# Performance work log

Hardware: AMD Instinct MI355X
Metric: run time of the kernel (lower is better)

Reference implementation:

```python
import jax, jax.numpy as jnp
import numpy as np


def setup_inputs() -> dict:
    key = jax.random.key(0)
    k1, k2 = jax.random.split(key)
    B, C, H, W = 8, 64, 64, 64
    x = jax.random.normal(k1, (B, C, H, W), dtype=jnp.float32)
    stdv = 1.0 / np.sqrt(C)
    weight = jax.random.uniform(k2, (C, C), dtype=jnp.float32, minval=-stdv, maxval=stdv)
    return {"x": x, "weight": weight}


def reference(x, weight):
    B, C, H, W = x.shape
    N = H * W
    xf = x.reshape(B, C, N)            # [B, C, N]
    g_x = jnp.transpose(xf, (0, 2, 1))  # [B, N, C] (also theta_x)
    # f[b, i, j] = sum_c x[b, c, i] * x[b, c, j]
    f = jnp.einsum('bic,bcj->bij', g_x, xf)  # [B, N, N]
    adj = jax.nn.softmax(f, axis=-1)
    support = jnp.einsum('bnc,cd->bnd', g_x, weight)  # [B, N, C]
    y = jnp.einsum('bij,bjc->bic', adj, support)      # [B, N, C]
    y = jnp.transpose(y, (0, 2, 1)).reshape(B, C, H, W)
    return y + x
```

## Files before the change

### kernel.cpp

```cpp
#include <hip/hip_runtime.h>
#include <stdint.h>


#define NTOK 4096
#define CCH  64

typedef float v4f __attribute__((ext_vector_type(4)));
typedef __bf16 v8bf __attribute__((ext_vector_type(8)));
typedef unsigned short v8us __attribute__((ext_vector_type(8)));

__device__ __forceinline__ unsigned short f2bf(float f) {
    union { float f; unsigned int u; } c; c.f = f;
    unsigned int r = c.u + 0x7fffu + ((c.u >> 16) & 1u);
    return (unsigned short)(r >> 16);
}

__device__ __forceinline__ v8bf ld8(const unsigned short* p) {
    union { v8us s; v8bf b; } u;
    u.s = *(const v8us*)p;
    return u.b;
}

__device__ __forceinline__ unsigned int pkbf(float a, float b) {
    union { float f; unsigned int u; } ua, ub; ua.f = a; ub.f = b;
    return __builtin_amdgcn_perm(ub.u, ua.u, 0x07060302u);
}

__device__ __forceinline__ void gload_lds16(const void* g, void* l) {
    __builtin_amdgcn_global_load_lds(
        (const __attribute__((address_space(1))) unsigned int*)g,
        (__attribute__((address_space(3))) unsigned int*)l,
        16, 0, 0);
}

__global__ __launch_bounds__(256) void prep_kernel(
    const float* __restrict__ x,
    const float* __restrict__ w,
    unsigned short* __restrict__ xT,
    unsigned short* __restrict__ sT)
{
    __shared__ float Xf[64 * 65];

    const int tid  = threadIdx.x;
    const int lane = tid & 63;
    const int wv   = __builtin_amdgcn_readfirstlane(tid >> 6);
    const int b    = blockIdx.y;
    const int n0   = blockIdx.x * 64;

    const float* xb = x + (size_t)b * CCH * NTOK + n0 + lane;
    #pragma unroll
    for (int k = 0; k < 16; ++k) {
        const int c = wv * 16 + k;
        Xf[c * 65 + lane] = xb[(size_t)c * NTOK];
    }
    __syncthreads();

    {
        const int n  = tid >> 2;
        const int c0 = (tid & 3) * 16;
        unsigned int pk[8];
        #pragma unroll
        for (int k = 0; k < 8; ++k) {
            const float a = Xf[(c0 + 2 * k) * 65 + n];
            const float c2 = Xf[(c0 + 2 * k + 1) * 65 + n];
            pk[k] = (unsigned int)f2bf(a) | ((unsigned int)f2bf(c2) << 16);
        }
        unsigned short* xtr = xT + ((size_t)b * NTOK + n0 + n) * CCH + c0;
        *(uint4*)(xtr)     = *(uint4*)(pk);
        *(uint4*)(xtr + 8) = *(uint4*)(pk + 4);
    }

    float acc[16];
    #pragma unroll
    for (int d = 0; d < 16; ++d) acc[d] = 0.f;

    #pragma unroll 4
    for (int c = 0; c < 64; ++c) {
        const float xc = Xf[c * 65 + lane];
        const float* wr = w + c * 64 + wv * 16;
        #pragma unroll
        for (int d = 0; d < 16; ++d) acc[d] = fmaf(xc, wr[d], acc[d]);
    }
    unsigned short* stb = sT + (size_t)b * CCH * NTOK + n0 + lane;
    #pragma unroll
    for (int d = 0; d < 16; ++d)
        stb[(size_t)(wv * 16 + d) * NTOK] = f2bf(acc[d]);
}

__global__ __launch_bounds__(256, 4) void flash_kernel(
    const unsigned short* __restrict__ xT,
    const unsigned short* __restrict__ sT,
    float* __restrict__ part_o,
    float* __restrict__ part_l,
    int nchunk, int chunk_len)
{
    __shared__ __align__(16) unsigned short Kt[64 * 64];
    __shared__ __align__(16) unsigned short Vt[64 * 64];
    __shared__ __align__(16) unsigned short Pt[4][32 * 64];

    const int tid  = threadIdx.x;
    const int w    = tid >> 6;
    const int lane = tid & 63;
    const int quad = lane >> 4;
    const int l16  = lane & 15;
    const int l7   = l16 & 7;
    const int b     = blockIdx.z;
    const int chunk = blockIdx.y;
    const int i0   = blockIdx.x * 128;
    const int irow = i0 + w * 32;
    const int jb   = chunk * chunk_len;

    const unsigned short* xTb = xT + (size_t)b * NTOK * CCH;
    const unsigned short* sTb = sT + (size_t)b * CCH * NTOK;

    const int srow = w * 8 + (lane >> 3);
    const int sc   = (lane & 7) ^ (lane >> 3);
    unsigned short* kd0 = Kt + w * 512;
    unsigned short* vd0 = Vt + w * 512;

    v8bf aq0[2], aq1[2];
    #pragma unroll
    for (int m = 0; m < 2; ++m) {
        const unsigned short* qr = xTb + (size_t)(irow + m * 16 + l16) * CCH + quad * 8;
        aq0[m] = ld8(qr);
        aq1[m] = ld8(qr + 32);
    }

    float negm[2];
    #pragma unroll
    for (int m = 0; m < 2; ++m) {
        float msq = 0.f;
        #pragma unroll
        for (int i = 0; i < 8; ++i) {
            float e0 = (float)aq0[m][i], e1 = (float)aq1[m][i];
            msq = fmaf(e0, e0, msq);
            msq = fmaf(e1, e1, msq);
        }
        msq += __shfl_xor(msq, 16);
        msq += __shfl_xor(msq, 32);
        negm[m] = -msq;
    }

    v4f o[2][4];
    #pragma unroll
    for (int m = 0; m < 2; ++m)
        #pragma unroll
        for (int ct = 0; ct < 4; ++ct) { o[m][ct][0]=0.f; o[m][ct][1]=0.f; o[m][ct][2]=0.f; o[m][ct][3]=0.f; }
    float rsum[2] = {0.f, 0.f};

    unsigned short* Pw = Pt[w];
    const int phalf = (quad & 1) * 4;
    const int pgq   = quad >> 1;

    for (int jj = 0; jj < chunk_len; jj += 64) {
        const int j0 = jb + jj;

        gload_lds16(xTb + (size_t)(j0 + srow) * CCH + sc * 8,       kd0);
        gload_lds16(xTb + (size_t)(j0 + 32 + srow) * CCH + sc * 8,  kd0 + 2048);
        gload_lds16(sTb + (size_t)srow * NTOK + j0 + sc * 8,        vd0);
        gload_lds16(sTb + (size_t)(32 + srow) * NTOK + j0 + sc * 8, vd0 + 2048);
        __syncthreads();

        #pragma unroll
        for (int jt = 0; jt < 4; ++jt) {
            const int krow = 16 * jt + l16;
            const unsigned short* kb = Kt + krow * 64;
            const int c0 = quad ^ (krow & 7);
            v8bf bk0 = ld8(kb + c0 * 8);
            v8bf bk1 = ld8(kb + (c0 ^ 4) * 8);
            #pragma unroll
            for (int m = 0; m < 2; ++m) {
                v4f z; z[0]=0.f; z[1]=0.f; z[2]=0.f; z[3]=0.f;
                z = __builtin_amdgcn_mfma_f32_16x16x32_bf16(bk0, aq0[m], z, 0, 0, 0);
                z = __builtin_amdgcn_mfma_f32_16x16x32_bf16(bk1, aq1[m], z, 0, 0, 0);
                const float p0 = __expf(z[0] + negm[m]);
                const float p1 = __expf(z[1] + negm[m]);
                const float p2 = __expf(z[2] + negm[m]);
                const float p3 = __expf(z[3] + negm[m]);
                rsum[m] += (p0 + p1) + (p2 + p3);
                uint2 pk; pk.x = pkbf(p0, p1); pk.y = pkbf(p2, p3);
                const int pos = (2 * jt + pgq) ^ l7;
                *(uint2*)(Pw + (m * 16 + l16) * 64 + pos * 8 + phalf) = pk;
            }
        }

        v8bf pb0[2], pb1[2];
        #pragma unroll
        for (int m = 0; m < 2; ++m) {
            const unsigned short* pr = Pw + (m * 16 + l16) * 64;
            const int p0c = quad ^ l7;
            pb0[m] = ld8(pr + p0c * 8);
            pb1[m] = ld8(pr + (p0c ^ 4) * 8);
        }

        #pragma unroll
        for (int ct = 0; ct < 4; ++ct) {
            const int vrow = 16 * ct + l16;
            const unsigned short* vb = Vt + vrow * 64;
            const int c0 = quad ^ (vrow & 7);
            v8bf bv0 = ld8(vb + c0 * 8);
            v8bf bv1 = ld8(vb + (c0 ^ 4) * 8);
            #pragma unroll
            for (int m = 0; m < 2; ++m) {
                o[m][ct] = __builtin_amdgcn_mfma_f32_16x16x32_bf16(bv0, pb0[m], o[m][ct], 0, 0, 0);
                o[m][ct] = __builtin_amdgcn_mfma_f32_16x16x32_bf16(bv1, pb1[m], o[m][ct], 0, 0, 0);
            }
        }
        __syncthreads();
    }

    const size_t pbase = (size_t)(b * nchunk + chunk) * NTOK + irow;
    #pragma unroll
    for (int m = 0; m < 2; ++m) {
        float t = rsum[m];
        t += __shfl_xor(t, 16);
        t += __shfl_xor(t, 32);
        if (quad == 0) part_l[pbase + m * 16 + l16] = t;
    }
    float* po = part_o + pbase * 64;
    #pragma unroll
    for (int m = 0; m < 2; ++m)
        #pragma unroll
        for (int ct = 0; ct < 4; ++ct)
            *(v4f*)(po + (size_t)(m * 16 + l16) * 64 + ct * 16 + quad * 4) = o[m][ct];
}

__global__ __launch_bounds__(256, 2) void combine_kernel(
    const float* __restrict__ part_o,
    const float* __restrict__ part_l,
    const float* __restrict__ x,
    float* __restrict__ out,
    int nchunk)
{
    __shared__ float Of[64 * 65];
    const int tid = threadIdx.x;
    const int b = blockIdx.y;
    const int i0 = blockIdx.x * 64;
    const int row = tid >> 2;
    const int seg = tid & 3;

    float acc[16];
    #pragma unroll
    for (int k = 0; k < 16; ++k) acc[k] = 0.f;
    float lt = 0.f;

    for (int ch = 0; ch < nchunk; ++ch) {
        const size_t base = (size_t)(b * nchunk + ch) * NTOK + i0 + row;
        lt += part_l[base];
        const float* po = part_o + base * 64 + seg * 16;
        #pragma unroll
        for (int k = 0; k < 4; ++k) {
            float4 v = *(const float4*)(po + k * 4);
            acc[k*4+0] += v.x; acc[k*4+1] += v.y; acc[k*4+2] += v.z; acc[k*4+3] += v.w;
        }
    }
    const float inv = 1.f / lt;
    #pragma unroll
    for (int k = 0; k < 16; ++k) Of[row * 65 + seg * 16 + k] = acc[k] * inv;
    __syncthreads();

    const int c    = tid >> 2;
    const int part = tid & 3;
    const float* xrow = x   + ((size_t)b * CCH + c) * NTOK + i0 + part * 16;
    float*       orow = out + ((size_t)b * CCH + c) * NTOK + i0 + part * 16;
    #pragma unroll
    for (int i4 = 0; i4 < 4; ++i4) {
        float4 xv = *(const float4*)(xrow + i4 * 4);
        float4 ov;
        ov.x = Of[(part * 16 + i4 * 4 + 0) * 65 + c] + xv.x;
        ov.y = Of[(part * 16 + i4 * 4 + 1) * 65 + c] + xv.y;
        ov.z = Of[(part * 16 + i4 * 4 + 2) * 65 + c] + xv.z;
        ov.w = Of[(part * 16 + i4 * 4 + 3) * 65 + c] + xv.w;
        *(float4*)(orow + i4 * 4) = ov;
    }
}

extern "C" void kernel_launch(void* const* d_in, const int* in_sizes, int n_in,
                              void* d_out, int out_size, void* d_ws, size_t ws_size,
                              hipStream_t stream) {
    const float* x = (const float*)d_in[0];
    const float* w = (const float*)d_in[1];
    float* out = (float*)d_out;

    const size_t xT_elems = (size_t)8 * NTOK * CCH;
    unsigned short* xT = (unsigned short*)d_ws;
    unsigned short* sT = xT + xT_elems;
    char* rest = (char*)d_ws + 2 * xT_elems * sizeof(unsigned short);

    int KS = 4;
    while (KS > 1) {
        size_t need = 2 * xT_elems * sizeof(unsigned short)
                    + (size_t)KS * ((size_t)8 * NTOK * CCH * 4 + (size_t)8 * NTOK * 4);
        if (need <= ws_size) break;
        KS >>= 1;
    }
    float* part_o = (float*)rest;
    float* part_l = (float*)(rest + (size_t)KS * 8 * NTOK * CCH * 4);

    dim3 gp(64, 8);
    prep_kernel<<<gp, 256, 0, stream>>>(x, w, xT, sT);
    dim3 gf(32, KS, 8);
    flash_kernel<<<gf, 256, 0, stream>>>(xT, sT, part_o, part_l, KS, NTOK / KS);
    dim3 gc(64, 8);
    combine_kernel<<<gc, 256, 0, stream>>>(part_o, part_l, x, out, KS);
}
```

Before: 125.9 us.

## Double query rows per wave, move row sums to MFMA, use exp2

Each wave now handles 64 query rows instead of 32, so each K/V tile loaded into LDS is reused across twice as many rows and the grid halves. Row sums of P are now computed with an extra MFMA against a ones vector rather than VALU adds plus shuffles, and exp is rewritten as exp2 with a fused LOG2E multiply. The combine kernel is templated on the chunk count so its loop fully unrolls. In exchange, register and LDS pressure rise (occupancy hint drops from 4 to 2), the grid has fewer blocks, and the row sums now come from bf16-rounded P values.

```diff
diff --git a/kernel.cpp b/kernel.cpp
--- a/kernel.cpp
+++ b/kernel.cpp
@@ -4,6 +4,7 @@
 
 #define NTOK 4096
 #define CCH  64
+#define LOG2E 1.44269504088896340736f
 
 typedef float v4f __attribute__((ext_vector_type(4)));
 typedef __bf16 v8bf __attribute__((ext_vector_type(8)));
@@ -87,7 +88,7 @@
         stb[(size_t)(wv * 16 + d) * NTOK] = f2bf(acc[d]);
 }
 
-__global__ __launch_bounds__(256, 4) void flash_kernel(
+__global__ __launch_bounds__(256, 2) void flash_kernel(
     const unsigned short* __restrict__ xT,
     const unsigned short* __restrict__ sT,
     float* __restrict__ part_o,
@@ -96,7 +97,7 @@
 {
     __shared__ __align__(16) unsigned short Kt[64 * 64];
     __shared__ __align__(16) unsigned short Vt[64 * 64];
-    __shared__ __align__(16) unsigned short Pt[4][32 * 64];
+    __shared__ __align__(16) unsigned short Pt[4][64 * 64];
 
     const int tid  = threadIdx.x;
     const int w    = tid >> 6;
@@ -106,8 +107,8 @@
     const int l7   = l16 & 7;
     const int b     = blockIdx.z;
     const int chunk = blockIdx.y;
-    const int i0   = blockIdx.x * 128;
-    const int irow = i0 + w * 32;
+    const int i0   = blockIdx.x * 256;
+    const int irow = i0 + w * 64;
     const int jb   = chunk * chunk_len;
 
     const unsigned short* xTb = xT + (size_t)b * NTOK * CCH;
@@ -118,17 +119,17 @@
     unsigned short* kd0 = Kt + w * 512;
     unsigned short* vd0 = Vt + w * 512;
 
-    v8bf aq0[2], aq1[2];
-    #pragma unroll
-    for (int m = 0; m < 2; ++m) {
+    v8bf aq0[4], aq1[4];
+    #pragma unroll
+    for (int m = 0; m < 4; ++m) {
         const unsigned short* qr = xTb + (size_t)(irow + m * 16 + l16) * CCH + quad * 8;
         aq0[m] = ld8(qr);
         aq1[m] = ld8(qr + 32);
     }
 
-    float negm[2];
-    #pragma unroll
-    for (int m = 0; m < 2; ++m) {
+    float negml2[4];
+    #pragma unroll
+    for (int m = 0; m < 4; ++m) {
         float msq = 0.f;
         #pragma unroll
         for (int i = 0; i < 8; ++i) {
@@ -138,15 +139,21 @@
         }
         msq += __shfl_xor(msq, 16);
         msq += __shfl_xor(msq, 32);
-        negm[m] = -msq;
-    }
-
-    v4f o[2][4];
-    #pragma unroll
-    for (int m = 0; m < 2; ++m)
+        negml2[m] = -msq * LOG2E;
+    }
+
+    v8bf ones;
+    #pragma unroll
+    for (int i = 0; i < 8; ++i) ones[i] = (__bf16)1.0f;
+
+    v4f o[4][4];
+    v4f lsum[4];
+    #pragma unroll
+    for (int m = 0; m < 4; ++m) {
+        lsum[m][0]=0.f; lsum[m][1]=0.f; lsum[m][2]=0.f; lsum[m][3]=0.f;
         #pragma unroll
         for (int ct = 0; ct < 4; ++ct) { o[m][ct][0]=0.f; o[m][ct][1]=0.f; o[m][ct][2]=0.f; o[m][ct][3]=0.f; }
-    float rsum[2] = {0.f, 0.f};
+    }
 
     unsigned short* Pw = Pt[w];
     const int phalf = (quad & 1) * 4;
@@ -169,28 +176,29 @@
             v8bf bk0 = ld8(kb + c0 * 8);
             v8bf bk1 = ld8(kb + (c0 ^ 4) * 8);
             #pragma unroll
-            for (int m = 0; m < 2; ++m) {
+            for (int m = 0; m < 4; ++m) {
                 v4f z; z[0]=0.f; z[1]=0.f; z[2]=0.f; z[3]=0.f;
                 z = __builtin_amdgcn_mfma_f32_16x16x32_bf16(bk0, aq0[m], z, 0, 0, 0);
                 z = __builtin_amdgcn_mfma_f32_16x16x32_bf16(bk1, aq1[m], z, 0, 0, 0);
-                const float p0 = __expf(z[0] + negm[m]);
-                const float p1 = __expf(z[1] + negm[m]);
-                const float p2 = __expf(z[2] + negm[m]);
-                const float p3 = __expf(z[3] + negm[m]);
-                rsum[m] += (p0 + p1) + (p2 + p3);
+                const float p0 = exp2f(fmaf(z[0], LOG2E, negml2[m]));
+                const float p1 = exp2f(fmaf(z[1], LOG2E, negml2[m]));
+                const float p2 = exp2f(fmaf(z[2], LOG2E, negml2[m]));
+                const float p3 = exp2f(fmaf(z[3], LOG2E, negml2[m]));
                 uint2 pk; pk.x = pkbf(p0, p1); pk.y = pkbf(p2, p3);
                 const int pos = (2 * jt + pgq) ^ l7;
                 *(uint2*)(Pw + (m * 16 + l16) * 64 + pos * 8 + phalf) = pk;
             }
         }
 
-        v8bf pb0[2], pb1[2];
-        #pragma unroll
-        for (int m = 0; m < 2; ++m) {
+        v8bf pb0[4], pb1[4];
+        #pragma unroll
+        for (int m = 0; m < 4; ++m) {
             const unsigned short* pr = Pw + (m * 16 + l16) * 64;
             const int p0c = quad ^ l7;
             pb0[m] = ld8(pr + p0c * 8);
             pb1[m] = ld8(pr + (p0c ^ 4) * 8);
+            lsum[m] = __builtin_amdgcn_mfma_f32_16x16x32_bf16(ones, pb0[m], lsum[m], 0, 0, 0);
+            lsum[m] = __builtin_amdgcn_mfma_f32_16x16x32_bf16(ones, pb1[m], lsum[m], 0, 0, 0);
         }
 
         #pragma unroll
@@ -201,7 +209,7 @@
             v8bf bv0 = ld8(vb + c0 * 8);
             v8bf bv1 = ld8(vb + (c0 ^ 4) * 8);
             #pragma unroll
-            for (int m = 0; m < 2; ++m) {
+            for (int m = 0; m < 4; ++m) {
                 o[m][ct] = __builtin_amdgcn_mfma_f32_16x16x32_bf16(bv0, pb0[m], o[m][ct], 0, 0, 0);
                 o[m][ct] = __builtin_amdgcn_mfma_f32_16x16x32_bf16(bv1, pb1[m], o[m][ct], 0, 0, 0);
             }
@@ -211,26 +219,22 @@
 
     const size_t pbase = (size_t)(b * nchunk + chunk) * NTOK + irow;
     #pragma unroll
-    for (int m = 0; m < 2; ++m) {
-        float t = rsum[m];
-        t += __shfl_xor(t, 16);
-        t += __shfl_xor(t, 32);
-        if (quad == 0) part_l[pbase + m * 16 + l16] = t;
-    }
+    for (int m = 0; m < 4; ++m)
+        if (quad == 0) part_l[pbase + m * 16 + l16] = lsum[m][0];
     float* po = part_o + pbase * 64;
     #pragma unroll
-    for (int m = 0; m < 2; ++m)
+    for (int m = 0; m < 4; ++m)
         #pragma unroll
         for (int ct = 0; ct < 4; ++ct)
             *(v4f*)(po + (size_t)(m * 16 + l16) * 64 + ct * 16 + quad * 4) = o[m][ct];
 }
 
+template <int KS_>
 __global__ __launch_bounds__(256, 2) void combine_kernel(
     const float* __restrict__ part_o,
     const float* __restrict__ part_l,
     const float* __restrict__ x,
-    float* __restrict__ out,
-    int nchunk)
+    float* __restrict__ out)
 {
     __shared__ float Of[64 * 65];
     const int tid = threadIdx.x;
@@ -244,8 +248,9 @@
     for (int k = 0; k < 16; ++k) acc[k] = 0.f;
     float lt = 0.f;
 
-    for (int ch = 0; ch < nchunk; ++ch) {
-        const size_t base = (size_t)(b * nchunk + ch) * NTOK + i0 + row;
+    #pragma unroll
+    for (int ch = 0; ch < KS_; ++ch) {
+        const size_t base = (size_t)(b * KS_ + ch) * NTOK + i0 + row;
         lt += part_l[base];
         const float* po = part_o + base * 64 + seg * 16;
         #pragma unroll
@@ -299,8 +304,10 @@
 
     dim3 gp(64, 8);
     prep_kernel<<<gp, 256, 0, stream>>>(x, w, xT, sT);
-    dim3 gf(32, KS, 8);
+    dim3 gf(16, KS, 8);
     flash_kernel<<<gf, 256, 0, stream>>>(xT, sT, part_o, part_l, KS, NTOK / KS);
     dim3 gc(64, 8);
-    combine_kernel<<<gc, 256, 0, stream>>>(part_o, part_l, x, out, KS);
-}
+    if (KS == 4)      combine_kernel<4><<<gc, 256, 0, stream>>>(part_o, part_l, x, out);
+    else if (KS == 2) combine_kernel<2><<<gc, 256, 0, stream>>>(part_o, part_l, x, out);
+    else              combine_kernel<1><<<gc, 256, 0, stream>>>(part_o, part_l, x, out);
+}
```

After: 139.2 us. +10.6%, slower.
